# Kernel optimization log

Measured on AMD Instinct MI355X. Metric: run time of the kernel, lower is better.

The kernel has to match this reference:

```python
import jax, jax.numpy as jnp
import numpy as np

N_PHOTONS = 20_000_000
HEX_R = 24  # axial hex grid radius -> 3R^2+3R+1 = 1801 pixels
SQRT3 = 3.0 ** 0.5


def _build_sensor():
    # Build pointy-top hex pixel centers on an axial grid (replicates hex_centers input),
    # then replicate HexagonalSensor.__init__ lookup-table construction in numpy.
    size = 1.0
    qs, rs = [], []
    for q in range(-HEX_R, HEX_R + 1):
        for r in range(max(-HEX_R, -q - HEX_R), min(HEX_R, -q + HEX_R) + 1):
            qs.append(q); rs.append(r)
    q = np.array(qs, dtype=np.float64); r = np.array(rs, dtype=np.float64)
    centers = np.stack([size * SQRT3 * (q + r / 2.0), size * 1.5 * r], axis=-1)
    n_pixels = centers.shape[0]
    diff = centers[:, None, :] - centers[None, :, :]
    d = np.sqrt((diff ** 2).sum(-1))
    np.fill_diagonal(d, np.inf)
    hex_size = float(d.min() / SQRT3)
    cx, cy = centers[:, 0], centers[:, 1]
    qa = (SQRT3 / 3.0 * cx - cy / 3.0) / hex_size
    ra = (2.0 / 3.0) * cy / hex_size
    q_offset = float(qa[0] - np.round(qa[0]))
    r_offset = float(ra[0] - np.round(ra[0]))
    q_grid = np.round(qa - q_offset).astype(np.int32)
    r_grid = np.round(ra - r_offset).astype(np.int32)
    q_min = int(q_grid.min()); r_min = int(r_grid.min())
    lookup = np.full((int(q_grid.max()) - q_min + 1, int(r_grid.max()) - r_min + 1), -1, dtype=np.int32)
    lookup[q_grid - q_min, r_grid - r_min] = np.arange(n_pixels)
    return hex_size, q_offset, r_offset, q_min, r_min, n_pixels, jnp.asarray(lookup)


def setup_inputs() -> dict:
    key = jax.random.key(0)
    kx, ky, kv = jax.random.split(key, 3)
    hex_size, q_off, r_off, q_min, r_min, n_pixels, lookup = _build_sensor()
    extent = 45.0  # camera footprint (~sqrt(3)*R + margin) so some photons miss (tests masking)
    x = jax.random.uniform(kx, (N_PHOTONS,), minval=-extent, maxval=extent, dtype=jnp.float32)
    y = jax.random.uniform(ky, (N_PHOTONS,), minval=-extent, maxval=extent, dtype=jnp.float32)
    values = jax.random.uniform(kv, (N_PHOTONS,), dtype=jnp.float32)
    return {"x": x, "y": y, "values": values, "lookup_table": lookup,
            "hex_size": hex_size, "q_offset": q_off, "r_offset": r_off,
            "q_min": q_min, "r_min": r_min, "n_pixels": n_pixels}


def _axial_round(q, r):
    s = -q - r
    qr, rr, sr = jnp.round(q), jnp.round(r), jnp.round(s)
    qd, rd, sd = jnp.abs(qr - q), jnp.abs(rr - r), jnp.abs(sr - s)
    qr2 = jnp.where((qd > rd) & (qd > sd), -rr - sr, qr)
    rr2 = jnp.where((rd > qd) & (rd > sd), -qr - sr, rr)
    return qr2, rr2


def reference(x, y, values, lookup_table, hex_size, q_offset, r_offset, q_min, r_min, n_pixels):
    # Cartesian -> axial hex coords
    q = (SQRT3 / 3.0 * x - y / 3.0) / hex_size
    r = (2.0 / 3.0) * y / hex_size
    qg, rg = _axial_round(q - q_offset, r - r_offset)
    q_idx = qg.astype(jnp.int32) - q_min
    r_idx = rg.astype(jnp.int32) - r_min
    Q, R = lookup_table.shape
    in_bounds = (q_idx >= 0) & (q_idx < Q) & (r_idx >= 0) & (r_idx < R)
    pixel_idx = lookup_table[q_idx.clip(0, Q - 1), r_idx.clip(0, R - 1)]
    valid = in_bounds & (pixel_idx >= 0)
    pixel_idx = jnp.where(valid, pixel_idx, 0)
    vals = jnp.where(valid, values, jnp.zeros((), values.dtype))
    return jax.ops.segment_sum(vals, pixel_idx, num_segments=n_pixels)
```

## Files before the change

### kernel.cpp

```cpp
#include <hip/hip_runtime.h>
#include <math.h>


typedef float f32x4 __attribute__((ext_vector_type(4)));

#define BIN_BLOCKS  512
#define BIN_THREADS 1024
#define RED_GROUP   32

__global__ void hex_zero_kernel(float* __restrict__ p, int n) {
    int i = blockIdx.x * blockDim.x + threadIdx.x;
    if (i < n) p[i] = 0.0f;
}

__global__ __launch_bounds__(256) void hex_reduce_kernel(
    const float* __restrict__ partials, float* __restrict__ out,
    int n_pixels, int nrows)
{
    int pix = blockIdx.x * blockDim.x + threadIdx.x;
    if (pix >= n_pixels) return;
    int r0 = blockIdx.y * RED_GROUP;
    int r1 = min(r0 + RED_GROUP, nrows);
    float s = 0.0f;
    const float* p = partials + (size_t)r0 * n_pixels + pix;
    #pragma unroll 8
    for (int r = r0; r < r1; ++r) {
        s += *p;
        p += n_pixels;
    }
    atomicAdd(&out[pix], s);
}

__global__ __launch_bounds__(BIN_THREADS) void hex_bin_kernel(
    const float* __restrict__ x,
    const float* __restrict__ y,
    const float* __restrict__ vals,
    const float* __restrict__ hex_size_p,
    const float* __restrict__ q_off_p,
    const float* __restrict__ r_off_p,
    const int*   __restrict__ q_min_p,
    const int*   __restrict__ r_min_p,
    int Rh, int n_pixels, int n_photons,
    float* __restrict__ flush_dst,
    int flush_mode)
{
    extern __shared__ float hist[];
    for (int i = threadIdx.x; i < n_pixels; i += blockDim.x) hist[i] = 0.0f;
    __syncthreads();

    const float inv_h = 1.0f / hex_size_p[0];
    const float A  = 0.57735026918962576f * inv_h;
    const float Bn = -(0.33333333333333333f * inv_h);
    const float C  = 0.66666666666666667f * inv_h;
    const float qc = -q_off_p[0];
    const float rc = -r_off_p[0];
    const int   qmin = q_min_p[0];
    const int   rmin = r_min_p[0];

    const unsigned twoR = (unsigned)(2 * Rh);
    const int Rp1 = Rh + 1;

    auto process = [&](float xf, float yf, float vf) {
        float q = fmaf(A, xf, fmaf(Bn, yf, qc));
        float r = fmaf(C, yf, rc);
        float t = q + r;
        float qr = rintf(q);
        float rr = rintf(r);
        float tr = rintf(t);
        float qd = fabsf(qr - q);
        float rd = fabsf(rr - r);
        float td = fabsf(tr - t);
        float q2 = (qd > rd && qd > td) ? (tr - rr) : qr;
        float r2 = (rd > qd && rd > td) ? (tr - qr) : rr;
        int qi = (int)q2 - qmin;
        int ri = (int)r2 - rmin;
        int d  = qi + ri;
        if ((unsigned)qi <= twoR && (unsigned)ri <= twoR &&
            (unsigned)(d - Rh) <= twoR) {
            int u  = max(qi - Rh, 0);
            int p  = qi * Rp1 + ((qi * qi - qi) >> 1) + d - Rh - u * u;
            atomicAdd(&hist[p], vf);
        }
    };

    const int n4 = n_photons >> 2;
    const f32x4* __restrict__ px = (const f32x4*)x;
    const f32x4* __restrict__ py = (const f32x4*)y;
    const f32x4* __restrict__ pv = (const f32x4*)vals;

    const int C4 = (n4 + gridDim.x - 1) / gridDim.x;
    const int g0 = blockIdx.x * C4;
    const int g1 = min(g0 + C4, n4);

    int g = g0 + threadIdx.x;
    f32x4 xa, ya, va;
    if (g < g1) {
        xa = __builtin_nontemporal_load(&px[g]);
        ya = __builtin_nontemporal_load(&py[g]);
        va = __builtin_nontemporal_load(&pv[g]);
    }
    while (g < g1) {
        int gn = g + blockDim.x;
        f32x4 nx, ny, nv;
        bool has_next = gn < g1;
        if (has_next) {
            nx = __builtin_nontemporal_load(&px[gn]);
            ny = __builtin_nontemporal_load(&py[gn]);
            nv = __builtin_nontemporal_load(&pv[gn]);
        }
        process(xa.x, ya.x, va.x);
        process(xa.y, ya.y, va.y);
        process(xa.z, ya.z, va.z);
        process(xa.w, ya.w, va.w);
        if (has_next) { xa = nx; ya = ny; va = nv; }
        g = gn;
    }

    {
        int t0 = (n4 << 2) + blockIdx.x * blockDim.x + threadIdx.x;
        int ts = gridDim.x * blockDim.x;
        for (int t = t0; t < n_photons; t += ts)
            process(x[t], y[t], vals[t]);
    }

    __syncthreads();
    if (flush_mode == 2) {
        float* dst = flush_dst + (size_t)blockIdx.x * n_pixels;
        for (int k = threadIdx.x; k < n_pixels; k += blockDim.x)
            dst[k] = hist[k];
    } else {
        for (int k = threadIdx.x; k < n_pixels; k += blockDim.x) {
            float h = hist[k];
            if (h != 0.0f) atomicAdd(&flush_dst[k], h);
        }
    }
}

extern "C" void kernel_launch(void* const* d_in, const int* in_sizes, int n_in,
                              void* d_out, int out_size, void* d_ws, size_t ws_size,
                              hipStream_t stream) {
    const float* x      = (const float*)d_in[0];
    const float* y      = (const float*)d_in[1];
    const float* vals   = (const float*)d_in[2];
    const float* hexs   = (const float*)d_in[4];
    const float* qoff   = (const float*)d_in[5];
    const float* roff   = (const float*)d_in[6];
    const int*   qmin   = (const int*)d_in[7];
    const int*   rmin   = (const int*)d_in[8];

    const int n_photons = in_sizes[0];
    const int lut_elems = in_sizes[3];
    const int Q  = (int)(0.5 + sqrt((double)lut_elems));
    const int Rh = (Q - 1) / 2;
    const int n_pixels = out_size;

    float* out = (float*)d_out;
    float* partials = (float*)d_ws;

    const size_t lds_bytes = (size_t)n_pixels * sizeof(float);
    const size_t part_elems = (size_t)BIN_BLOCKS * (size_t)n_pixels;

    if (ws_size >= part_elems * sizeof(float)) {
        hex_zero_kernel<<<(n_pixels + 255) / 256, 256, 0, stream>>>(out, n_pixels);
        hex_bin_kernel<<<BIN_BLOCKS, BIN_THREADS, lds_bytes, stream>>>(
            x, y, vals, hexs, qoff, roff, qmin, rmin,
            Rh, n_pixels, n_photons, partials, 2);
        dim3 rgrid((n_pixels + 255) / 256, BIN_BLOCKS / RED_GROUP);
        hex_reduce_kernel<<<rgrid, 256, 0, stream>>>(
            partials, out, n_pixels, BIN_BLOCKS);
    } else {
        hex_zero_kernel<<<(n_pixels + 255) / 256, 256, 0, stream>>>(out, n_pixels);
        hex_bin_kernel<<<BIN_BLOCKS, BIN_THREADS, lds_bytes, stream>>>(
            x, y, vals, hexs, qoff, roff, qmin, rmin,
            Rh, n_pixels, n_photons, out, 0);
    }
}
```

Before: 74.04 us.

## Stream photon tiles into LDS with async global_load_lds double buffering

```diff
diff --git a/kernel.cpp b/kernel.cpp
--- a/kernel.cpp
+++ b/kernel.cpp
@@ -4,8 +4,11 @@
 
 typedef float f32x4 __attribute__((ext_vector_type(4)));
 
-#define BIN_BLOCKS  512
-#define BIN_THREADS 1024
+#define BIN_BLOCKS  1280
+#define BIN_THREADS 256
+#define TILE_G      256
+#define HIST_F      1808
+#define BUF_F       3072
 #define RED_GROUP   32
 
 __global__ void hex_zero_kernel(float* __restrict__ p, int n) {
@@ -44,8 +47,8 @@
     float* __restrict__ flush_dst,
     int flush_mode)
 {
-    extern __shared__ float hist[];
-    for (int i = threadIdx.x; i < n_pixels; i += blockDim.x) hist[i] = 0.0f;
+    extern __shared__ float lds[];
+    for (int i = threadIdx.x; i < HIST_F; i += blockDim.x) lds[i] = 0.0f;
     __syncthreads();
 
     const float inv_h = 1.0f / hex_size_p[0];
@@ -79,7 +82,7 @@
             (unsigned)(d - Rh) <= twoR) {
             int u  = max(qi - Rh, 0);
             int p  = qi * Rp1 + ((qi * qi - qi) >> 1) + d - Rh - u * u;
-            atomicAdd(&hist[p], vf);
+            atomicAdd(&lds[p], vf);
         }
     };
 
@@ -91,33 +94,73 @@
     const int C4 = (n4 + gridDim.x - 1) / gridDim.x;
     const int g0 = blockIdx.x * C4;
     const int g1 = min(g0 + C4, n4);
-
-    int g = g0 + threadIdx.x;
-    f32x4 xa, ya, va;
-    if (g < g1) {
-        xa = __builtin_nontemporal_load(&px[g]);
-        ya = __builtin_nontemporal_load(&py[g]);
-        va = __builtin_nontemporal_load(&pv[g]);
-    }
-    while (g < g1) {
-        int gn = g + blockDim.x;
-        f32x4 nx, ny, nv;
-        bool has_next = gn < g1;
-        if (has_next) {
-            nx = __builtin_nontemporal_load(&px[gn]);
-            ny = __builtin_nontemporal_load(&py[gn]);
-            nv = __builtin_nontemporal_load(&pv[gn]);
-        }
+    const int Cg = g1 - g0;
+    const int T  = (Cg > 0) ? (Cg / TILE_G) : 0;
+
+    const int tid = (int)threadIdx.x;
+
+    auto stage = [&](int bsel, int tile) {
+        int g = g0 + tile * TILE_G + tid;
+        int base = HIST_F + bsel * BUF_F + ((tid >> 6) << 8);
+        int ub = __builtin_amdgcn_readfirstlane(base);
+        __builtin_amdgcn_global_load_lds(
+            (const __attribute__((address_space(1))) void*)&px[g],
+            (__attribute__((address_space(3))) void*)&lds[ub + 0],    16, 0, 0);
+        __builtin_amdgcn_global_load_lds(
+            (const __attribute__((address_space(1))) void*)&py[g],
+            (__attribute__((address_space(3))) void*)&lds[ub + 1024], 16, 0, 0);
+        __builtin_amdgcn_global_load_lds(
+            (const __attribute__((address_space(1))) void*)&pv[g],
+            (__attribute__((address_space(3))) void*)&lds[ub + 2048], 16, 0, 0);
+    };
+
+    if (T > 0) {
+        stage(0, 0);
+        if (T > 1) {
+            stage(1, 1);
+            asm volatile("s_waitcnt vmcnt(3)" ::: "memory");
+        } else {
+            asm volatile("s_waitcnt vmcnt(0)" ::: "memory");
+        }
+        __builtin_amdgcn_sched_barrier(0);
+        __builtin_amdgcn_s_barrier();
+
+        for (int t = 0; t < T; ++t) {
+            int cur = t & 1;
+            int bb = HIST_F + cur * BUF_F + tid * 4;
+            f32x4 xa = *(const f32x4*)&lds[bb + 0];
+            f32x4 ya = *(const f32x4*)&lds[bb + 1024];
+            f32x4 va = *(const f32x4*)&lds[bb + 2048];
+            process(xa.x, ya.x, va.x);
+            process(xa.y, ya.y, va.y);
+            process(xa.z, ya.z, va.z);
+            process(xa.w, ya.w, va.w);
+            __builtin_amdgcn_s_barrier();
+            if (t + 1 < T) {
+                if (t + 2 < T) {
+                    stage(cur, t + 2);
+                    asm volatile("s_waitcnt vmcnt(3)" ::: "memory");
+                } else {
+                    asm volatile("s_waitcnt vmcnt(0)" ::: "memory");
+                }
+                __builtin_amdgcn_sched_barrier(0);
+                __builtin_amdgcn_s_barrier();
+            }
+        }
+    }
+
+    for (int g = g0 + T * TILE_G + tid; g < g1; g += TILE_G) {
+        f32x4 xa = px[g];
+        f32x4 ya = py[g];
+        f32x4 va = pv[g];
         process(xa.x, ya.x, va.x);
         process(xa.y, ya.y, va.y);
         process(xa.z, ya.z, va.z);
         process(xa.w, ya.w, va.w);
-        if (has_next) { xa = nx; ya = ny; va = nv; }
-        g = gn;
     }
 
     {
-        int t0 = (n4 << 2) + blockIdx.x * blockDim.x + threadIdx.x;
+        int t0 = (n4 << 2) + blockIdx.x * blockDim.x + tid;
         int ts = gridDim.x * blockDim.x;
         for (int t = t0; t < n_photons; t += ts)
             process(x[t], y[t], vals[t]);
@@ -126,11 +169,11 @@
     __syncthreads();
     if (flush_mode == 2) {
         float* dst = flush_dst + (size_t)blockIdx.x * n_pixels;
-        for (int k = threadIdx.x; k < n_pixels; k += blockDim.x)
-            dst[k] = hist[k];
+        for (int k = tid; k < n_pixels; k += blockDim.x)
+            dst[k] = lds[k];
     } else {
-        for (int k = threadIdx.x; k < n_pixels; k += blockDim.x) {
-            float h = hist[k];
+        for (int k = tid; k < n_pixels; k += blockDim.x) {
+            float h = lds[k];
             if (h != 0.0f) atomicAdd(&flush_dst[k], h);
         }
     }
@@ -157,7 +200,7 @@
     float* out = (float*)d_out;
     float* partials = (float*)d_ws;
 
-    const size_t lds_bytes = (size_t)n_pixels * sizeof(float);
+    const size_t lds_bytes = (size_t)(HIST_F + 2 * BUF_F) * sizeof(float);
     const size_t part_elems = (size_t)BIN_BLOCKS * (size_t)n_pixels;
 
     if (ws_size >= part_elems * sizeof(float)) {
```

Result: slower. 94.94 us (+28.2%).

## Drop zero kernel, reduce partials directly, process eight photons per thread iteration

Applied to the files above, without the earlier changes.

```diff
diff --git a/kernel.cpp b/kernel.cpp
--- a/kernel.cpp
+++ b/kernel.cpp
@@ -6,29 +6,26 @@
 
 #define BIN_BLOCKS  512
 #define BIN_THREADS 1024
-#define RED_GROUP   32
 
 __global__ void hex_zero_kernel(float* __restrict__ p, int n) {
     int i = blockIdx.x * blockDim.x + threadIdx.x;
     if (i < n) p[i] = 0.0f;
 }
 
-__global__ __launch_bounds__(256) void hex_reduce_kernel(
+__global__ __launch_bounds__(256) void hex_reduce_direct(
     const float* __restrict__ partials, float* __restrict__ out,
     int n_pixels, int nrows)
 {
     int pix = blockIdx.x * blockDim.x + threadIdx.x;
     if (pix >= n_pixels) return;
-    int r0 = blockIdx.y * RED_GROUP;
-    int r1 = min(r0 + RED_GROUP, nrows);
     float s = 0.0f;
-    const float* p = partials + (size_t)r0 * n_pixels + pix;
-    #pragma unroll 8
-    for (int r = r0; r < r1; ++r) {
+    const float* p = partials + pix;
+    #pragma unroll 16
+    for (int r = 0; r < nrows; ++r) {
         s += *p;
         p += n_pixels;
     }
-    atomicAdd(&out[pix], s);
+    out[pix] = s;
 }
 
 __global__ __launch_bounds__(BIN_THREADS) void hex_bin_kernel(
@@ -84,40 +81,56 @@
     };
 
     const int n4 = n_photons >> 2;
+    const int n8 = n4 >> 1;
     const f32x4* __restrict__ px = (const f32x4*)x;
     const f32x4* __restrict__ py = (const f32x4*)y;
     const f32x4* __restrict__ pv = (const f32x4*)vals;
 
-    const int C4 = (n4 + gridDim.x - 1) / gridDim.x;
-    const int g0 = blockIdx.x * C4;
-    const int g1 = min(g0 + C4, n4);
+    const int P  = (n8 + gridDim.x - 1) / gridDim.x;
+    const int j0 = blockIdx.x * P;
+    const int j1 = min(j0 + P, n8);
+    const int BS = blockDim.x;
 
-    int g = g0 + threadIdx.x;
-    f32x4 xa, ya, va;
-    if (g < g1) {
-        xa = __builtin_nontemporal_load(&px[g]);
-        ya = __builtin_nontemporal_load(&py[g]);
-        va = __builtin_nontemporal_load(&pv[g]);
+    int j = j0 + threadIdx.x;
+    f32x4 xa, xb, ya, yb, va, vb;
+    if (j < j1) {
+        int a = 2 * j, b = a + 1;
+        xa = __builtin_nontemporal_load(&px[a]);
+        xb = __builtin_nontemporal_load(&px[b]);
+        ya = __builtin_nontemporal_load(&py[a]);
+        yb = __builtin_nontemporal_load(&py[b]);
+        va = __builtin_nontemporal_load(&pv[a]);
+        vb = __builtin_nontemporal_load(&pv[b]);
     }
-    while (g < g1) {
-        int gn = g + blockDim.x;
-        f32x4 nx, ny, nv;
-        bool has_next = gn < g1;
+    while (j < j1) {
+        int jn = j + BS;
+        f32x4 nxa, nxb, nya, nyb, nva, nvb;
+        bool has_next = jn < j1;
         if (has_next) {
-            nx = __builtin_nontemporal_load(&px[gn]);
-            ny = __builtin_nontemporal_load(&py[gn]);
-            nv = __builtin_nontemporal_load(&pv[gn]);
+            int a = 2 * jn, b = a + 1;
+            nxa = __builtin_nontemporal_load(&px[a]);
+            nxb = __builtin_nontemporal_load(&px[b]);
+            nya = __builtin_nontemporal_load(&py[a]);
+            nyb = __builtin_nontemporal_load(&py[b]);
+            nva = __builtin_nontemporal_load(&pv[a]);
+            nvb = __builtin_nontemporal_load(&pv[b]);
         }
         process(xa.x, ya.x, va.x);
         process(xa.y, ya.y, va.y);
         process(xa.z, ya.z, va.z);
         process(xa.w, ya.w, va.w);
-        if (has_next) { xa = nx; ya = ny; va = nv; }
-        g = gn;
+        process(xb.x, yb.x, vb.x);
+        process(xb.y, yb.y, vb.y);
+        process(xb.z, yb.z, vb.z);
+        process(xb.w, yb.w, vb.w);
+        if (has_next) {
+            xa = nxa; xb = nxb; ya = nya; yb = nyb; va = nva; vb = nvb;
+        }
+        j = jn;
     }
 
     {
-        int t0 = (n4 << 2) + blockIdx.x * blockDim.x + threadIdx.x;
+        int t0 = (n8 << 3) + blockIdx.x * blockDim.x + threadIdx.x;
         int ts = gridDim.x * blockDim.x;
         for (int t = t0; t < n_photons; t += ts)
             process(x[t], y[t], vals[t]);
@@ -161,12 +174,10 @@
     const size_t part_elems = (size_t)BIN_BLOCKS * (size_t)n_pixels;
 
     if (ws_size >= part_elems * sizeof(float)) {
-        hex_zero_kernel<<<(n_pixels + 255) / 256, 256, 0, stream>>>(out, n_pixels);
         hex_bin_kernel<<<BIN_BLOCKS, BIN_THREADS, lds_bytes, stream>>>(
             x, y, vals, hexs, qoff, roff, qmin, rmin,
             Rh, n_pixels, n_photons, partials, 2);
-        dim3 rgrid((n_pixels + 255) / 256, BIN_BLOCKS / RED_GROUP);
-        hex_reduce_kernel<<<rgrid, 256, 0, stream>>>(
+        hex_reduce_direct<<<(n_pixels + 255) / 256, 256, 0, stream>>>(
             partials, out, n_pixels, BIN_BLOCKS);
     } else {
         hex_zero_kernel<<<(n_pixels + 255) / 256, 256, 0, stream>>>(out, n_pixels);
```

Result: slower. 82.52 us (+11.4%).
